# Performance work log

Hardware: AMD Instinct MI355X
Metric: run time of the kernel (lower is better)

Reference implementation:

```python
import jax, jax.numpy as jnp
import numpy as np

B, S, H_SZ = 1, 2048, 2048
E, K, KVH, D = 8, 2, 16, 128      # experts, top_k, kv heads, head_dim
QH = K * KVH                       # 32 query heads
QSZ = KVH * D                      # 2048 per-expert q/o size


def setup_inputs() -> dict:
    key = jax.random.key(0)
    ks = jax.random.split(key, 6)
    hidden_states = jax.random.normal(ks[0], (B, S, H_SZ), jnp.float32)
    causal = jnp.tril(jnp.ones((S, S), dtype=bool))
    attention_bias = jnp.where(causal, 0.0, -1e9).astype(jnp.float32)[None, None]  # [1,1,S,S]
    inv_freq = 1.0 / (10000.0 ** (jnp.arange(0, D, 2, dtype=jnp.float32) / D))     # [D/2]
    ang = jnp.arange(S, dtype=jnp.float32)[:, None] * inv_freq[None, :]            # [S,D/2]
    cos, sin = jnp.cos(ang), jnp.sin(ang)
    router_w = jax.random.normal(ks[1], (E, H_SZ), jnp.float32) * 0.02
    q_w = jax.random.normal(ks[2], (E, QSZ, H_SZ), jnp.float32) * 0.02
    o_w = jax.random.normal(ks[3], (E, H_SZ, QSZ), jnp.float32) * 0.02
    kv_w = jax.random.normal(ks[4], (2 * QSZ, H_SZ), jnp.float32) * 0.02
    bias = jax.random.normal(ks[5], (H_SZ,), jnp.float32) * 0.02
    return {"hidden_states": hidden_states, "attention_bias": attention_bias,
            "cos": cos, "sin": sin, "router_w": router_w, "q_w": q_w,
            "o_w": o_w, "kv_w": kv_w, "bias": bias}


def _rope(x, cos, sin):
    # x: [b,s,h,d]; half-rotation rotary, cos/sin: [s,d/2]
    d2 = x.shape[-1] // 2
    x1, x2 = x[..., :d2], x[..., d2:]
    c = cos[None, :, None, :]
    s = sin[None, :, None, :]
    return jnp.concatenate([x1 * c - x2 * s, x1 * s + x2 * c], axis=-1)


def reference(hidden_states, attention_bias, cos, sin, router_w, q_w, o_w, kv_w, bias):
    # ---- router: top-k + softmax over top-k logits ----
    logits = jnp.einsum('bsh,eh->bse', hidden_states, router_w)         # [b,s,E]
    top_vals, sel = jax.lax.top_k(logits, K)                            # [b,s,K]
    gates = jax.nn.softmax(top_vals, axis=-1)                           # [b,s,K]
    # ---- per-expert Q projections (dense, as in original), gather selected ----
    q_all = jnp.einsum('bsh,eqh->bseq', hidden_states, q_w)             # [b,s,E,QSZ]
    q_sel = jnp.take_along_axis(q_all, sel[..., None], axis=2)          # [b,s,K,QSZ]
    # slots -> kv-major head layout: [b,s,K,KVH,D] -> [b,s,KVH,K,D] -> [b,s,QH,D]
    q = q_sel.reshape(B, S, K, KVH, D).transpose(0, 1, 3, 2, 4).reshape(B, S, QH, D)
    # ---- shared K/V ----
    kv = jnp.einsum('bsh,oh->bso', hidden_states, kv_w)                 # [b,s,2*QSZ]
    k_st, v_st = jnp.split(kv, 2, axis=-1)
    k_st = k_st.reshape(B, S, KVH, D)
    v_st = v_st.reshape(B, S, KVH, D)
    # ---- rotary ----
    q = _rope(q, cos, sin)
    k_st = _rope(k_st, cos, sin)
    # ---- GQA attention (group size K; kv-major query layout matches repeat) ----
    k_rep = jnp.repeat(k_st, K, axis=2)                                 # [b,s,QH,D]
    v_rep = jnp.repeat(v_st, K, axis=2)
    scale = D ** -0.5
    scores = jnp.einsum('bqhd,bkhd->bhqk', q, k_rep) * scale + attention_bias
    probs = jax.nn.softmax(scores, axis=-1)
    attn = jnp.einsum('bhqk,bkhd->bqhd', probs, v_rep)                  # [b,s,QH,D]
    # back to slot-major: [b,s,KVH,K,D] -> [b,s,K,KVH,D] -> [b,s,K,QSZ]
    attn4 = attn.reshape(B, S, KVH, K, D).transpose(0, 1, 3, 2, 4).reshape(B, S, K, QSZ)
    # ---- per-expert O projections, masked + gated sum (as in original) ----
    out = jnp.zeros((B, S, H_SZ), hidden_states.dtype)
    for e in range(E):
        o_e = jnp.einsum('bskq,hq->bskh', attn4, o_w[e])                # [b,s,K,H]
        m = (sel == e).astype(hidden_states.dtype) * gates              # [b,s,K]
        out = out + jnp.einsum('bsk,bskh->bsh', m, o_e)
    return out + bias
```

## Files before the change

### kernel.cpp

```cpp
#include <hip/hip_runtime.h>
#include <hip/hip_bf16.h>
#include <stdint.h>

#define S_LEN 2048
#define HSZ 2048
#define NE 8
#define TOPK 2
#define NKVH 16
#define HD 128
#define NQH 32
#define QSZ 2048

typedef __attribute__((ext_vector_type(8))) __bf16 bf16x8;
typedef __attribute__((ext_vector_type(4))) float f32x4;

#define BM 128
#define BN 128
#define BK 64

__device__ __forceinline__ void gload_lds16(const void* g, void* l) {
  __builtin_amdgcn_global_load_lds((__attribute__((address_space(1))) void*)g,
                                   (__attribute__((address_space(3))) void*)l, 16, 0, 0);
}

__device__ __forceinline__ bf16x8 pack8(float4 a, float4 b) {
  bf16x8 r;
  r[0] = (__bf16)a.x; r[1] = (__bf16)a.y; r[2] = (__bf16)a.z; r[3] = (__bf16)a.w;
  r[4] = (__bf16)b.x; r[5] = (__bf16)b.y; r[6] = (__bf16)b.z; r[7] = (__bf16)b.w;
  return r;
}

__global__ __launch_bounds__(256) void cast_kernel(const float* __restrict__ src,
                                                   __bf16* __restrict__ dst, long n) {
  long i0 = ((long)blockIdx.x * 256 + threadIdx.x) * 4;
  long stride = (long)gridDim.x * 256 * 4;
  for (long i = i0; i < n; i += stride) {
    float4 v = *(const float4*)(src + i);
    unsigned short a = __builtin_bit_cast(unsigned short, (__bf16)v.x);
    unsigned short b = __builtin_bit_cast(unsigned short, (__bf16)v.y);
    unsigned short c = __builtin_bit_cast(unsigned short, (__bf16)v.z);
    unsigned short d = __builtin_bit_cast(unsigned short, (__bf16)v.w);
    uint2 o;
    o.x = (unsigned)a | ((unsigned)b << 16);
    o.y = (unsigned)c | ((unsigned)d << 16);
    *(uint2*)(dst + i) = o;
  }
}

__global__ __launch_bounds__(256) void router_kernel(const float* __restrict__ hs,
                                                     const float* __restrict__ rw,
                                                     int* __restrict__ sel,
                                                     float* __restrict__ gates) {
  const int s = blockIdx.x * 4 + (threadIdx.x >> 6);
  const int lane = threadIdx.x & 63;
  const float* row = hs + (size_t)s * HSZ;
  float acc[NE];
#pragma unroll
  for (int e = 0; e < NE; ++e) acc[e] = 0.f;
  for (int j = lane; j < HSZ; j += 64) {
    float x = row[j];
#pragma unroll
    for (int e = 0; e < NE; ++e) acc[e] += x * rw[e * HSZ + j];
  }
#pragma unroll
  for (int e = 0; e < NE; ++e) {
#pragma unroll
    for (int off = 32; off > 0; off >>= 1) acc[e] += __shfl_xor(acc[e], off);
  }
  if (lane == 0) {
    int i0 = 0; float v0 = acc[0];
#pragma unroll
    for (int e = 1; e < NE; ++e) if (acc[e] > v0) { v0 = acc[e]; i0 = e; }
    int i1 = -1; float v1 = -1e30f;
#pragma unroll
    for (int e = 0; e < NE; ++e) if (e != i0 && acc[e] > v1) { v1 = acc[e]; i1 = e; }
    float ge = __expf(v1 - v0);
    float den = 1.f + ge;
    sel[s * 2] = i0; sel[s * 2 + 1] = i1;
    gates[s * 2] = 1.f / den; gates[s * 2 + 1] = ge / den;
  }
}

__global__ void bucket_kernel(const int* __restrict__ sel, int* __restrict__ pair_list,
                              int* __restrict__ expert_off) {
  __shared__ int cnt[NE], base[NE];
  const int t = threadIdx.x;
  if (t < NE) cnt[t] = 0;
  __syncthreads();
  for (int p2 = t; p2 < S_LEN * TOPK; p2 += 256) atomicAdd(&cnt[sel[p2]], 1);
  __syncthreads();
  if (t == 0) {
    int run = 0;
#pragma unroll
    for (int e = 0; e < NE; ++e) { base[e] = run; expert_off[e] = run; run += cnt[e]; }
    expert_off[NE] = run;
  }
  __syncthreads();
  for (int p2 = t; p2 < S_LEN * TOPK; p2 += 256) {
    int pos = atomicAdd(&base[sel[p2]], 1);
    pair_list[pos] = p2;
  }
}

template <int MODE>
__global__ __launch_bounds__(256, 2) void gemm_kernel(const __bf16* __restrict__ A_src,
                                                      const float* __restrict__ B_src,
                                                      const int* __restrict__ pair_list,
                                                      const int* __restrict__ expert_off,
                                                      const float* __restrict__ gates,
                                                      __bf16* __restrict__ out_bf,
                                                      __bf16* __restrict__ out_vT,
                                                      float* __restrict__ out_f32) {
  constexpr int KD = 2048;
  constexpr int NT = KD / BK;
  const int n0 = blockIdx.x * BN;
  const int m0 = blockIdx.y * BM;
  const int e = blockIdx.z;
  int start = 0, cntv = S_LEN;
  if constexpr (MODE != 0) {
    start = expert_off[e];
    cntv = expert_off[e + 1] - start;
    if (m0 >= cntv) return;
  }
  const float* Bb = B_src + (size_t)e * QSZ * HSZ;
  __shared__ __attribute__((aligned(16))) __bf16 As[2][BM * BK];
  __shared__ __attribute__((aligned(16))) __bf16 Bs[2][BN * BK];
  __shared__ const __bf16* a_rows[BM];
  __shared__ int row_pair[BM];
  const int t = threadIdx.x;
  if (t < BM) {
    if constexpr (MODE == 0) {
      a_rows[t] = A_src + (size_t)(m0 + t) * KD;
      row_pair[t] = 0;
    } else {
      int idx = m0 + t;
      bool valid = idx < cntv;
      int pp = pair_list[start + (valid ? idx : 0)];
      row_pair[t] = valid ? pp : -1;
      size_t arow = (MODE == 1) ? (size_t)(pp >> 1) : (size_t)pp;
      a_rows[t] = A_src + arow * (size_t)KD;
    }
  }
  __syncthreads();

  const int lane = t & 63, w = t >> 6;
  const int wr = (w >> 1) * 64, wc = (w & 1) * 64;
  const int lr = lane & 15, g = lane >> 4;
  const int xa = lr & 7;

  const __bf16* a_srow[4];
  int a_soff[4];
#pragma unroll
  for (int i = 0; i < 4; ++i) {
    const int c = t + i * 256;
    const int row = c >> 3, win = c & 7;
    a_srow[i] = a_rows[row];
    a_soff[i] = (win ^ (row & 7)) * 8;
  }

  const int brow = t >> 2;
  const int bq = t & 3;
  const float* bp0 = Bb + (size_t)(n0 + brow) * KD + bq * 16;
  const float* bp1 = bp0 + (size_t)64 * KD;
  const int c0 = (2 * bq) ^ (brow & 7);
  const int c1 = (2 * bq + 1) ^ (brow & 7);
  const int bo00 = brow * BK + c0 * 8, bo01 = brow * BK + c1 * 8;
  const int bo10 = (brow + 64) * BK + c0 * 8, bo11 = (brow + 64) * BK + c1 * 8;

  f32x4 acc[4][4];
#pragma unroll
  for (int m = 0; m < 4; ++m)
#pragma unroll
    for (int n = 0; n < 4; ++n) acc[m][n] = (f32x4)0.f;

  float4 cA0 = *(const float4*)(bp0), cA1 = *(const float4*)(bp0 + 4);
  float4 cA2 = *(const float4*)(bp0 + 8), cA3 = *(const float4*)(bp0 + 12);
  float4 cB0 = *(const float4*)(bp1), cB1 = *(const float4*)(bp1 + 4);
  float4 cB2 = *(const float4*)(bp1 + 8), cB3 = *(const float4*)(bp1 + 12);
  __builtin_amdgcn_sched_barrier(0);
#pragma unroll
  for (int i = 0; i < 4; ++i)
    gload_lds16(a_srow[i] + a_soff[i], (char*)As[0] + (t + i * 256) * 16);
  __builtin_amdgcn_sched_barrier(0);

#pragma unroll 2
  for (int ti = 0; ti < NT; ++ti) {
    const int cur = ti & 1;
    *(bf16x8*)(&Bs[cur][bo00]) = pack8(cA0, cA1);
    *(bf16x8*)(&Bs[cur][bo01]) = pack8(cA2, cA3);
    *(bf16x8*)(&Bs[cur][bo10]) = pack8(cB0, cB1);
    *(bf16x8*)(&Bs[cur][bo11]) = pack8(cB2, cB3);
    asm volatile("s_waitcnt lgkmcnt(0)" ::: "memory");
    __builtin_amdgcn_s_barrier();

    if (ti + 1 < NT) {
      const int k1 = (ti + 1) * BK;
      cA0 = *(const float4*)(bp0 + k1); cA1 = *(const float4*)(bp0 + k1 + 4);
      cA2 = *(const float4*)(bp0 + k1 + 8); cA3 = *(const float4*)(bp0 + k1 + 12);
      cB0 = *(const float4*)(bp1 + k1); cB1 = *(const float4*)(bp1 + k1 + 4);
      cB2 = *(const float4*)(bp1 + k1 + 8); cB3 = *(const float4*)(bp1 + k1 + 12);
      __builtin_amdgcn_sched_barrier(0);
#pragma unroll
      for (int i = 0; i < 4; ++i)
        gload_lds16(a_srow[i] + k1 + a_soff[i], (char*)As[cur ^ 1] + (t + i * 256) * 16);
      asm volatile("s_waitcnt vmcnt(12)" ::: "memory");
    } else {
      asm volatile("s_waitcnt vmcnt(0)" ::: "memory");
    }
    __builtin_amdgcn_sched_barrier(0);

#pragma unroll
    for (int kk = 0; kk < BK; kk += 32) {
      bf16x8 af[4], bfv[4];
#pragma unroll
      for (int m = 0; m < 4; ++m)
        af[m] = *(const bf16x8*)(&As[cur][(wr + m * 16 + lr) * BK + (((kk >> 3) + g) ^ xa) * 8]);
#pragma unroll
      for (int n = 0; n < 4; ++n)
        bfv[n] = *(const bf16x8*)(&Bs[cur][(wc + n * 16 + lr) * BK + (((kk >> 3) + g) ^ xa) * 8]);
#pragma unroll
      for (int m = 0; m < 4; ++m)
#pragma unroll
        for (int n = 0; n < 4; ++n)
          acc[m][n] = __builtin_amdgcn_mfma_f32_16x16x32_bf16(af[m], bfv[n], acc[m][n], 0, 0, 0);
    }
    __builtin_amdgcn_sched_barrier(0);
  }

  const int lg = lane >> 4;
  if constexpr (MODE == 0) {
    if (n0 < 2048) {
#pragma unroll
      for (int m = 0; m < 4; ++m)
#pragma unroll
        for (int r = 0; r < 4; ++r) {
          const int row = wr + m * 16 + lg * 4 + r;
#pragma unroll
          for (int n = 0; n < 4; ++n) {
            const int col = n0 + wc + n * 16 + lr;
            out_bf[(size_t)(m0 + row) * 2048 + col] = (__bf16)acc[m][n][r];
          }
        }
    } else {
#pragma unroll
      for (int m = 0; m < 4; ++m) {
        const int sb = m0 + wr + m * 16 + lg * 4;
#pragma unroll
        for (int n = 0; n < 4; ++n) {
          const int cv = n0 + wc + n * 16 + lr - 2048;
          uint2 pk;
          unsigned short h0 = __builtin_bit_cast(unsigned short, (__bf16)acc[m][n][0]);
          unsigned short h1 = __builtin_bit_cast(unsigned short, (__bf16)acc[m][n][1]);
          unsigned short h2 = __builtin_bit_cast(unsigned short, (__bf16)acc[m][n][2]);
          unsigned short h3 = __builtin_bit_cast(unsigned short, (__bf16)acc[m][n][3]);
          pk.x = (unsigned)h0 | ((unsigned)h1 << 16);
          pk.y = (unsigned)h2 | ((unsigned)h3 << 16);
          *(uint2*)(out_vT + (size_t)cv * S_LEN + sb) = pk;
        }
      }
    }
  } else {
#pragma unroll
    for (int m = 0; m < 4; ++m) {
#pragma unroll
      for (int r = 0; r < 4; ++r) {
        const int row = wr + m * 16 + lg * 4 + r;
        const int pp = row_pair[row];
        if (pp < 0) continue;
        if constexpr (MODE == 1) {
#pragma unroll
          for (int n = 0; n < 4; ++n) {
            const int col = n0 + wc + n * 16 + lr;
            out_bf[(size_t)pp * QSZ + col] = (__bf16)acc[m][n][r];
          }
        } else {
          const float gt = gates[pp];
#pragma unroll
          for (int n = 0; n < 4; ++n) {
            const int col = n0 + wc + n * 16 + lr;
            out_f32[(size_t)pp * HSZ + col] = acc[m][n][r] * gt;
          }
        }
      }
    }
  }
}

__global__ __launch_bounds__(256) void rope_q_kernel(const __bf16* __restrict__ q_lin,
                                                     const float* __restrict__ cosb,
                                                     const float* __restrict__ sinb,
                                                     __bf16* __restrict__ q_attn) {
  const int idx = blockIdx.x * 4 + (threadIdx.x >> 6);
  const int lane = threadIdx.x & 63;
  const int s = idx >> 5;
  const int h = idx & 31;
  const int kvh = h >> 1, k = h & 1;
  const __bf16* src = q_lin + ((size_t)s * 2 + k) * QSZ + kvh * HD;
  float x1 = (float)src[lane];
  float x2 = (float)src[lane + 64];
  float c = cosb[s * 64 + lane], sn = sinb[s * 64 + lane];
  __bf16* dst = q_attn + ((size_t)h * S_LEN + s) * HD;
  dst[lane] = (__bf16)(x1 * c - x2 * sn);
  dst[lane + 64] = (__bf16)(x1 * sn + x2 * c);
}

__global__ __launch_bounds__(256) void rope_k_kernel(const __bf16* __restrict__ kv_lin,
                                                     const float* __restrict__ cosb,
                                                     const float* __restrict__ sinb,
                                                     __bf16* __restrict__ k_attn) {
  const int idx = blockIdx.x * 4 + (threadIdx.x >> 6);
  const int lane = threadIdx.x & 63;
  const int s = idx >> 4;
  const int gq = idx & 15;
  const __bf16* ksrc = kv_lin + (size_t)s * 2048 + gq * HD;
  float x1 = (float)ksrc[lane], x2 = (float)ksrc[lane + 64];
  float c = cosb[s * 64 + lane], sn = sinb[s * 64 + lane];
  __bf16* kd = k_attn + ((size_t)gq * S_LEN + s) * HD;
  kd[lane] = (__bf16)(x1 * c - x2 * sn);
  kd[lane + 64] = (__bf16)(x1 * sn + x2 * c);
}

__global__ __launch_bounds__(256, 2) void attn_kernel(const __bf16* __restrict__ q_attn,
                                                      const __bf16* __restrict__ k_attn,
                                                      const __bf16* __restrict__ vT,
                                                      __bf16* __restrict__ attn4) {
  __shared__ __attribute__((aligned(16))) __bf16 Ks[2][64 * 128];
  __shared__ __attribute__((aligned(16))) __bf16 Vs[2][128 * 64];
  const int h = blockIdx.x;
  const int by = (blockIdx.y < 8) ? blockIdx.y : 23 - blockIdx.y;
  const int s0 = by * 128;
  const int t = threadIdx.x;
  const int lane = t & 63;
  const int w = t >> 6;
  const int g = lane >> 4;
  const int lr = lane & 15;
  const int kvh = h >> 1;

  int koff[4], voff[4];
#pragma unroll
  for (int i = 0; i < 4; ++i) {
    const int c = t + i * 256;
    const int kvL = c >> 4, w16 = c & 15;
    koff[i] = kvL * HD + ((w16 ^ (kvL & 7)) * 8);
    const int d = c >> 3, w8 = c & 7;
    voff[i] = d * S_LEN + ((w8 ^ (d & 7)) * 8);
  }
  const __bf16* Kb = k_attn + (size_t)kvh * S_LEN * HD;
  const __bf16* Vb = vT + (size_t)kvh * HD * S_LEN;

  auto stage = [&](int buf, int kv0) {
#pragma unroll
    for (int i = 0; i < 4; ++i) {
      const int c = t + i * 256;
      gload_lds16(Kb + (size_t)kv0 * HD + koff[i], (char*)Ks[buf] + c * 16);
      gload_lds16(Vb + (size_t)kv0 + voff[i], (char*)Vs[buf] + c * 16);
    }
  };

  bf16x8 qf[2][4];
#pragma unroll
  for (int m = 0; m < 2; ++m) {
    const __bf16* qbase = q_attn + ((size_t)h * S_LEN + s0 + w * 32 + m * 16 + lr) * HD;
#pragma unroll
    for (int ds = 0; ds < 4; ++ds) qf[m][ds] = *(const bf16x8*)(qbase + ds * 32 + g * 8);
  }

  float m_run[2] = {-1e30f, -1e30f}, l_run[2] = {0.f, 0.f};
  f32x4 acc[2][8];
#pragma unroll
  for (int m = 0; m < 2; ++m)
#pragma unroll
    for (int dt = 0; dt < 8; ++dt) acc[m][dt] = (f32x4)0.f;

  const int xr = (lr & 7) << 4;
  const int nt = 2 * by + 2;
  stage(0, 0);
  for (int ti = 0; ti < nt; ++ti) {
    const int cur = ti & 1;
    const int kv0 = ti * 64;
    __syncthreads();
    if (ti + 1 < nt) stage(cur ^ 1, kv0 + 64);

    f32x4 sc[2][4];
#pragma unroll
    for (int m = 0; m < 2; ++m)
#pragma unroll
      for (int b = 0; b < 4; ++b) sc[m][b] = (f32x4)0.f;
#pragma unroll
    for (int b = 0; b < 4; ++b) {
#pragma unroll
      for (int ds = 0; ds < 4; ++ds) {
        const bf16x8 kf = *(const bf16x8*)((const char*)Ks[cur] +
            (b * 16 + lr) * 256 + ((ds * 64 + g * 16) ^ xr));
        sc[0][b] = __builtin_amdgcn_mfma_f32_16x16x32_bf16(kf, qf[0][ds], sc[0][b], 0, 0, 0);
        sc[1][b] = __builtin_amdgcn_mfma_f32_16x16x32_bf16(kf, qf[1][ds], sc[1][b], 0, 0, 0);
      }
    }

    bf16x8 paf[2][2];
#pragma unroll
    for (int m = 0; m < 2; ++m) {
      const int qrow = s0 + w * 32 + m * 16 + lr;
      float p[4][4];
      float tmax = -1e30f;
#pragma unroll
      for (int b = 0; b < 4; ++b)
#pragma unroll
        for (int r = 0; r < 4; ++r) {
          const int kv = kv0 + b * 16 + g * 4 + r;
          float v = sc[m][b][r] * 0.08838834764831845f;
          if (kv > qrow) v = -1e30f;
          p[b][r] = v;
          tmax = fmaxf(tmax, v);
        }
      tmax = fmaxf(tmax, __shfl_xor(tmax, 16));
      tmax = fmaxf(tmax, __shfl_xor(tmax, 32));
      const float m_new = fmaxf(m_run[m], tmax);
      const float alpha = __expf(m_run[m] - m_new);
      float lsum = 0.f;
#pragma unroll
      for (int b = 0; b < 4; ++b)
#pragma unroll
        for (int r = 0; r < 4; ++r) {
          p[b][r] = __expf(p[b][r] - m_new);
          lsum += p[b][r];
        }
      lsum += __shfl_xor(lsum, 16);
      lsum += __shfl_xor(lsum, 32);
      l_run[m] = l_run[m] * alpha + lsum;
      m_run[m] = m_new;

      float ar[4];
#pragma unroll
      for (int r = 0; r < 4; ++r) ar[r] = __shfl(alpha, g * 4 + r);
#pragma unroll
      for (int dt = 0; dt < 8; ++dt)
#pragma unroll
        for (int r = 0; r < 4; ++r) acc[m][dt][r] *= ar[r];

#pragma unroll
      for (int half = 0; half < 2; ++half) {
        bf16x8 af;
#pragma unroll
        for (int j = 0; j < 8; ++j) {
          const int srcl = lr + 16 * ((g & 1) * 2 + (j >> 2));
          const float va = __shfl(p[half * 2][j & 3], srcl);
          const float vb = __shfl(p[half * 2 + 1][j & 3], srcl);
          af[j] = (__bf16)((g >> 1) ? vb : va);
        }
        paf[m][half] = af;
      }
    }

#pragma unroll
    for (int dt = 0; dt < 8; ++dt) {
      const char* vrow = (const char*)Vs[cur] + (dt * 16 + lr) * 128;
      const bf16x8 v0 = *(const bf16x8*)(vrow + ((g * 16) ^ xr));
      const bf16x8 v1 = *(const bf16x8*)(vrow + ((64 + g * 16) ^ xr));
      acc[0][dt] = __builtin_amdgcn_mfma_f32_16x16x32_bf16(paf[0][0], v0, acc[0][dt], 0, 0, 0);
      acc[0][dt] = __builtin_amdgcn_mfma_f32_16x16x32_bf16(paf[0][1], v1, acc[0][dt], 0, 0, 0);
      acc[1][dt] = __builtin_amdgcn_mfma_f32_16x16x32_bf16(paf[1][0], v0, acc[1][dt], 0, 0, 0);
      acc[1][dt] = __builtin_amdgcn_mfma_f32_16x16x32_bf16(paf[1][1], v1, acc[1][dt], 0, 0, 0);
    }
  }

#pragma unroll
  for (int m = 0; m < 2; ++m) {
    const float li = 1.f / l_run[m];
    float linv[4];
#pragma unroll
    for (int r = 0; r < 4; ++r) linv[r] = __shfl(li, g * 4 + r);
#pragma unroll
    for (int dt = 0; dt < 8; ++dt)
#pragma unroll
      for (int r = 0; r < 4; ++r) {
        const int qg = s0 + w * 32 + m * 16 + g * 4 + r;
        attn4[((size_t)qg * 2 + (h & 1)) * QSZ + kvh * HD + dt * 16 + lr] =
            (__bf16)(acc[m][dt][r] * linv[r]);
      }
  }
}

__global__ __launch_bounds__(256) void final_kernel(const float* __restrict__ o_tmp,
                                                    const float* __restrict__ bias,
                                                    float* __restrict__ out) {
  const size_t i = ((size_t)blockIdx.x * 256 + threadIdx.x) * 4;
  const int s = (int)(i >> 11);
  const int hcol = (int)(i & 2047);
  float4 a = *(const float4*)(o_tmp + ((size_t)s * 2) * HSZ + hcol);
  float4 b = *(const float4*)(o_tmp + ((size_t)s * 2 + 1) * HSZ + hcol);
  float4 bb = *(const float4*)(bias + hcol);
  float4 o;
  o.x = a.x + b.x + bb.x; o.y = a.y + b.y + bb.y;
  o.z = a.z + b.z + bb.z; o.w = a.w + b.w + bb.w;
  *(float4*)(out + i) = o;
}

extern "C" void kernel_launch(void* const* d_in, const int* in_sizes, int n_in,
                              void* d_out, int out_size, void* d_ws, size_t ws_size,
                              hipStream_t stream) {
  (void)in_sizes; (void)n_in; (void)out_size; (void)ws_size;
  const float* hs = (const float*)d_in[0];
  const float* cosb = (const float*)d_in[2];
  const float* sinb = (const float*)d_in[3];
  const float* rw = (const float*)d_in[4];
  const float* qw = (const float*)d_in[5];
  const float* ow = (const float*)d_in[6];
  const float* kvw = (const float*)d_in[7];
  const float* bias = (const float*)d_in[8];
  float* outp = (float*)d_out;

  char* base = (char*)d_ws;
  size_t off = 0;
  auto take = [&](size_t bytes) {
    char* r = base + off;
    off += (bytes + 255) & ~(size_t)255;
    return r;
  };
  __bf16* hid_bf  = (__bf16*)take((size_t)S_LEN * HSZ * 2);
  __bf16* k_attn  = (__bf16*)take((size_t)NKVH * S_LEN * HD * 2);
  __bf16* v_attnT = (__bf16*)take((size_t)NKVH * HD * S_LEN * 2);
  char* bufA = take((size_t)S_LEN * 4096 * 2);
  char* bufBC = take((size_t)S_LEN * TOPK * HSZ * 4);
  int* sel = (int*)take((size_t)S_LEN * TOPK * 4);
  float* gates = (float*)take((size_t)S_LEN * TOPK * 4);
  int* pair_list = (int*)take((size_t)S_LEN * TOPK * 4);
  int* expert_off = (int*)take((size_t)(NE + 1) * 4);

  __bf16* kv_lin = (__bf16*)bufA;
  __bf16* attn4 = (__bf16*)bufA;
  __bf16* q_lin = (__bf16*)bufBC;
  __bf16* q_attn = (__bf16*)(bufBC + (size_t)16 * 1024 * 1024);
  float* o_tmp = (float*)bufBC;

  cast_kernel<<<1024, 256, 0, stream>>>(hs, hid_bf, (long)S_LEN * HSZ);
  router_kernel<<<S_LEN / 4, 256, 0, stream>>>(hs, rw, sel, gates);
  bucket_kernel<<<1, 256, 0, stream>>>(sel, pair_list, expert_off);
  gemm_kernel<0><<<dim3(4096 / BN, S_LEN / BM, 1), 256, 0, stream>>>(
      hid_bf, kvw, nullptr, nullptr, nullptr, kv_lin, v_attnT, nullptr);
  rope_k_kernel<<<S_LEN * NKVH / 4, 256, 0, stream>>>(kv_lin, cosb, sinb, k_attn);
  gemm_kernel<1><<<dim3(QSZ / BN, 32, NE), 256, 0, stream>>>(
      hid_bf, qw, pair_list, expert_off, nullptr, q_lin, nullptr, nullptr);
  rope_q_kernel<<<S_LEN * NQH / 4, 256, 0, stream>>>(q_lin, cosb, sinb, q_attn);
  attn_kernel<<<dim3(NQH, 16), 256, 0, stream>>>(q_attn, k_attn, v_attnT, attn4);
  gemm_kernel<2><<<dim3(HSZ / BN, 32, NE), 256, 0, stream>>>(
      attn4, ow, pair_list, expert_off, gates, nullptr, nullptr, o_tmp);
  final_kernel<<<(S_LEN * HSZ / 4) / 256, 256, 0, stream>>>(o_tmp, bias, outp);
}
```

Measured before the change: 423.5 us.

## Split-K expert GEMMs, fuse Q rotary into attention, emit bf16 partials

The two expert GEMMs now split the K dimension in two across blockIdx.z and write bf16 partial results. The Q partials are summed and rotated inside the attention kernel, which removes the separate rope_q pass. The O partials are summed in the final kernel, so the fp32 o_tmp buffer is no longer needed. The GEMM tile depth drops from 64 to 32 and launch bounds ask for 4 blocks per SM to raise occupancy, at the cost of dropping the LDS XOR swizzle and the explicit vmcnt waits. The bf16 partial sums lose some precision, and the unswizzled layout may cause LDS bank conflicts.

```diff
diff --git a/kernel.cpp b/kernel.cpp
--- a/kernel.cpp
+++ b/kernel.cpp
@@ -16,7 +16,7 @@
 
 #define BM 128
 #define BN 128
-#define BK 64
+#define BK 32
 
 __device__ __forceinline__ void gload_lds16(const void* g, void* l) {
   __builtin_amdgcn_global_load_lds((__attribute__((address_space(1))) void*)g,
@@ -103,26 +103,26 @@
 }
 
 template <int MODE>
-__global__ __launch_bounds__(256, 2) void gemm_kernel(const __bf16* __restrict__ A_src,
-                                                      const float* __restrict__ B_src,
-                                                      const int* __restrict__ pair_list,
-                                                      const int* __restrict__ expert_off,
-                                                      const float* __restrict__ gates,
-                                                      __bf16* __restrict__ out_bf,
-                                                      __bf16* __restrict__ out_vT,
-                                                      float* __restrict__ out_f32) {
+__global__ __launch_bounds__(256, 4) void gemm_kernel(
+    const __bf16* __restrict__ A_src, const float* __restrict__ B_src,
+    const int* __restrict__ pair_list, const int* __restrict__ expert_off,
+    const float* __restrict__ gates, __bf16* __restrict__ out0,
+    __bf16* __restrict__ out_vT) {
   constexpr int KD = 2048;
-  constexpr int NT = KD / BK;
+  constexpr int NT = (MODE == 0) ? 64 : 32;
   const int n0 = blockIdx.x * BN;
   const int m0 = blockIdx.y * BM;
-  const int e = blockIdx.z;
-  int start = 0, cntv = S_LEN;
+  int kbase = 0, kz = 0, start = 0, cntv = S_LEN;
+  const float* Bb = B_src;
   if constexpr (MODE != 0) {
+    const int e = blockIdx.z >> 1;
+    kz = blockIdx.z & 1;
+    kbase = kz * 1024;
     start = expert_off[e];
     cntv = expert_off[e + 1] - start;
     if (m0 >= cntv) return;
-  }
-  const float* Bb = B_src + (size_t)e * QSZ * HSZ;
+    Bb = B_src + (size_t)e * QSZ * HSZ;
+  }
   __shared__ __attribute__((aligned(16))) __bf16 As[2][BM * BK];
   __shared__ __attribute__((aligned(16))) __bf16 Bs[2][BN * BK];
   __shared__ const __bf16* a_rows[BM];
@@ -138,7 +138,7 @@
       int pp = pair_list[start + (valid ? idx : 0)];
       row_pair[t] = valid ? pp : -1;
       size_t arow = (MODE == 1) ? (size_t)(pp >> 1) : (size_t)pp;
-      a_rows[t] = A_src + arow * (size_t)KD;
+      a_rows[t] = A_src + arow * (size_t)KD + kbase;
     }
   }
   __syncthreads();
@@ -146,26 +146,18 @@
   const int lane = t & 63, w = t >> 6;
   const int wr = (w >> 1) * 64, wc = (w & 1) * 64;
   const int lr = lane & 15, g = lane >> 4;
-  const int xa = lr & 7;
-
-  const __bf16* a_srow[4];
-  int a_soff[4];
-#pragma unroll
-  for (int i = 0; i < 4; ++i) {
+
+  const __bf16* a_srow[2];
+  int a_scol[2];
+#pragma unroll
+  for (int i = 0; i < 2; ++i) {
     const int c = t + i * 256;
-    const int row = c >> 3, win = c & 7;
-    a_srow[i] = a_rows[row];
-    a_soff[i] = (win ^ (row & 7)) * 8;
-  }
-
-  const int brow = t >> 2;
-  const int bq = t & 3;
-  const float* bp0 = Bb + (size_t)(n0 + brow) * KD + bq * 16;
-  const float* bp1 = bp0 + (size_t)64 * KD;
-  const int c0 = (2 * bq) ^ (brow & 7);
-  const int c1 = (2 * bq + 1) ^ (brow & 7);
-  const int bo00 = brow * BK + c0 * 8, bo01 = brow * BK + c1 * 8;
-  const int bo10 = (brow + 64) * BK + c0 * 8, bo11 = (brow + 64) * BK + c1 * 8;
+    a_srow[i] = a_rows[c >> 2];
+    a_scol[i] = (c & 3) * 8;
+  }
+
+  const float* bp = Bb + (size_t)(n0 + (t >> 1)) * KD + kbase + (t & 1) * 16;
+  const int bwo = (t >> 1) * BK + (t & 1) * 16;
 
   f32x4 acc[4][4];
 #pragma unroll
@@ -173,51 +165,42 @@
 #pragma unroll
     for (int n = 0; n < 4; ++n) acc[m][n] = (f32x4)0.f;
 
-  float4 cA0 = *(const float4*)(bp0), cA1 = *(const float4*)(bp0 + 4);
-  float4 cA2 = *(const float4*)(bp0 + 8), cA3 = *(const float4*)(bp0 + 12);
-  float4 cB0 = *(const float4*)(bp1), cB1 = *(const float4*)(bp1 + 4);
-  float4 cB2 = *(const float4*)(bp1 + 8), cB3 = *(const float4*)(bp1 + 12);
-  __builtin_amdgcn_sched_barrier(0);
-#pragma unroll
-  for (int i = 0; i < 4; ++i)
-    gload_lds16(a_srow[i] + a_soff[i], (char*)As[0] + (t + i * 256) * 16);
+  auto stageA = [&](int buf, int k0) {
+#pragma unroll
+    for (int i = 0; i < 2; ++i)
+      gload_lds16(a_srow[i] + k0 + a_scol[i], (char*)As[buf] + (t + i * 256) * 16);
+  };
+
+  float4 c0, c1, c2, c3;
+#define B_LOAD(KB)                                                           \
+  c0 = *(const float4*)(bp + (KB));     c1 = *(const float4*)(bp + (KB) + 4); \
+  c2 = *(const float4*)(bp + (KB) + 8); c3 = *(const float4*)(bp + (KB) + 12);
+
+  stageA(0, 0);
+  B_LOAD(0)
   __builtin_amdgcn_sched_barrier(0);
 
 #pragma unroll 2
   for (int ti = 0; ti < NT; ++ti) {
     const int cur = ti & 1;
-    *(bf16x8*)(&Bs[cur][bo00]) = pack8(cA0, cA1);
-    *(bf16x8*)(&Bs[cur][bo01]) = pack8(cA2, cA3);
-    *(bf16x8*)(&Bs[cur][bo10]) = pack8(cB0, cB1);
-    *(bf16x8*)(&Bs[cur][bo11]) = pack8(cB2, cB3);
+    *(bf16x8*)(&Bs[cur][bwo]) = pack8(c0, c1);
+    *(bf16x8*)(&Bs[cur][bwo + 8]) = pack8(c2, c3);
     asm volatile("s_waitcnt lgkmcnt(0)" ::: "memory");
     __builtin_amdgcn_s_barrier();
-
+    __builtin_amdgcn_sched_barrier(0);
     if (ti + 1 < NT) {
-      const int k1 = (ti + 1) * BK;
-      cA0 = *(const float4*)(bp0 + k1); cA1 = *(const float4*)(bp0 + k1 + 4);
-      cA2 = *(const float4*)(bp0 + k1 + 8); cA3 = *(const float4*)(bp0 + k1 + 12);
-      cB0 = *(const float4*)(bp1 + k1); cB1 = *(const float4*)(bp1 + k1 + 4);
-      cB2 = *(const float4*)(bp1 + k1 + 8); cB3 = *(const float4*)(bp1 + k1 + 12);
-      __builtin_amdgcn_sched_barrier(0);
-#pragma unroll
-      for (int i = 0; i < 4; ++i)
-        gload_lds16(a_srow[i] + k1 + a_soff[i], (char*)As[cur ^ 1] + (t + i * 256) * 16);
-      asm volatile("s_waitcnt vmcnt(12)" ::: "memory");
-    } else {
-      asm volatile("s_waitcnt vmcnt(0)" ::: "memory");
+      stageA(cur ^ 1, (ti + 1) * BK);
+      B_LOAD((ti + 1) * BK)
     }
     __builtin_amdgcn_sched_barrier(0);
-
-#pragma unroll
-    for (int kk = 0; kk < BK; kk += 32) {
+    {
       bf16x8 af[4], bfv[4];
 #pragma unroll
       for (int m = 0; m < 4; ++m)
-        af[m] = *(const bf16x8*)(&As[cur][(wr + m * 16 + lr) * BK + (((kk >> 3) + g) ^ xa) * 8]);
+        af[m] = *(const bf16x8*)(&As[cur][(wr + m * 16 + lr) * BK + g * 8]);
 #pragma unroll
       for (int n = 0; n < 4; ++n)
-        bfv[n] = *(const bf16x8*)(&Bs[cur][(wc + n * 16 + lr) * BK + (((kk >> 3) + g) ^ xa) * 8]);
+        bfv[n] = *(const bf16x8*)(&Bs[cur][(wc + n * 16 + lr) * BK + g * 8]);
 #pragma unroll
       for (int m = 0; m < 4; ++m)
 #pragma unroll
@@ -226,6 +209,7 @@
     }
     __builtin_amdgcn_sched_barrier(0);
   }
+#undef B_LOAD
 
   const int lg = lane >> 4;
   if constexpr (MODE == 0) {
@@ -238,7 +222,7 @@
 #pragma unroll
           for (int n = 0; n < 4; ++n) {
             const int col = n0 + wc + n * 16 + lr;
-            out_bf[(size_t)(m0 + row) * 2048 + col] = (__bf16)acc[m][n][r];
+            out0[(size_t)(m0 + row) * 2048 + col] = (__bf16)acc[m][n][r];
           }
         }
     } else {
@@ -260,6 +244,7 @@
       }
     }
   } else {
+    __bf16* outp = out0 + (size_t)kz * 4096 * 2048;
 #pragma unroll
     for (int m = 0; m < 4; ++m) {
 #pragma unroll
@@ -267,41 +252,16 @@
         const int row = wr + m * 16 + lg * 4 + r;
         const int pp = row_pair[row];
         if (pp < 0) continue;
-        if constexpr (MODE == 1) {
-#pragma unroll
-          for (int n = 0; n < 4; ++n) {
-            const int col = n0 + wc + n * 16 + lr;
-            out_bf[(size_t)pp * QSZ + col] = (__bf16)acc[m][n][r];
-          }
-        } else {
-          const float gt = gates[pp];
-#pragma unroll
-          for (int n = 0; n < 4; ++n) {
-            const int col = n0 + wc + n * 16 + lr;
-            out_f32[(size_t)pp * HSZ + col] = acc[m][n][r] * gt;
-          }
+        float gt = 1.f;
+        if constexpr (MODE == 2) gt = gates[pp];
+#pragma unroll
+        for (int n = 0; n < 4; ++n) {
+          const int col = n0 + wc + n * 16 + lr;
+          outp[(size_t)pp * 2048 + col] = (__bf16)(acc[m][n][r] * gt);
         }
       }
     }
   }
-}
-
-__global__ __launch_bounds__(256) void rope_q_kernel(const __bf16* __restrict__ q_lin,
-                                                     const float* __restrict__ cosb,
-                                                     const float* __restrict__ sinb,
-                                                     __bf16* __restrict__ q_attn) {
-  const int idx = blockIdx.x * 4 + (threadIdx.x >> 6);
-  const int lane = threadIdx.x & 63;
-  const int s = idx >> 5;
-  const int h = idx & 31;
-  const int kvh = h >> 1, k = h & 1;
-  const __bf16* src = q_lin + ((size_t)s * 2 + k) * QSZ + kvh * HD;
-  float x1 = (float)src[lane];
-  float x2 = (float)src[lane + 64];
-  float c = cosb[s * 64 + lane], sn = sinb[s * 64 + lane];
-  __bf16* dst = q_attn + ((size_t)h * S_LEN + s) * HD;
-  dst[lane] = (__bf16)(x1 * c - x2 * sn);
-  dst[lane + 64] = (__bf16)(x1 * sn + x2 * c);
 }
 
 __global__ __launch_bounds__(256) void rope_k_kernel(const __bf16* __restrict__ kv_lin,
@@ -320,9 +280,11 @@
   kd[lane + 64] = (__bf16)(x1 * sn + x2 * c);
 }
 
-__global__ __launch_bounds__(256, 2) void attn_kernel(const __bf16* __restrict__ q_attn,
+__global__ __launch_bounds__(256, 2) void attn_kernel(const __bf16* __restrict__ q_part,
                                                       const __bf16* __restrict__ k_attn,
                                                       const __bf16* __restrict__ vT,
+                                                      const float* __restrict__ cosb,
+                                                      const float* __restrict__ sinb,
                                                       __bf16* __restrict__ attn4) {
   __shared__ __attribute__((aligned(16))) __bf16 Ks[2][64 * 128];
   __shared__ __attribute__((aligned(16))) __bf16 Vs[2][128 * 64];
@@ -360,9 +322,29 @@
   bf16x8 qf[2][4];
 #pragma unroll
   for (int m = 0; m < 2; ++m) {
-    const __bf16* qbase = q_attn + ((size_t)h * S_LEN + s0 + w * 32 + m * 16 + lr) * HD;
-#pragma unroll
-    for (int ds = 0; ds < 4; ++ds) qf[m][ds] = *(const bf16x8*)(qbase + ds * 32 + g * 8);
+    const int qrow = s0 + w * 32 + m * 16 + lr;
+    const __bf16* p0 = q_part + (size_t)(qrow * 2 + (h & 1)) * QSZ + kvh * HD;
+    const __bf16* p1 = p0 + (size_t)4096 * 2048;
+    const float* cp = cosb + qrow * 64;
+    const float* sp = sinb + qrow * 64;
+#pragma unroll
+    for (int ds = 0; ds < 4; ++ds) {
+      const int d0 = ds * 32 + g * 8;
+      const int dl = d0 & 63;
+      const bf16x8 xa = *(const bf16x8*)(p0 + d0);
+      const bf16x8 xb = *(const bf16x8*)(p1 + d0);
+      const bf16x8 ya = *(const bf16x8*)(p0 + (d0 ^ 64));
+      const bf16x8 yb = *(const bf16x8*)(p1 + (d0 ^ 64));
+      bf16x8 o;
+#pragma unroll
+      for (int j = 0; j < 8; ++j) {
+        const float x = (float)xa[j] + (float)xb[j];
+        const float y = (float)ya[j] + (float)yb[j];
+        const float c = cp[dl + j], sn = sp[dl + j];
+        o[j] = (__bf16)((ds < 2) ? (x * c - y * sn) : (y * sn + x * c));
+      }
+      qf[m][ds] = o;
+    }
   }
 
   float m_run[2] = {-1e30f, -1e30f}, l_run[2] = {0.f, 0.f};
@@ -481,19 +463,23 @@
   }
 }
 
-__global__ __launch_bounds__(256) void final_kernel(const float* __restrict__ o_tmp,
+__global__ __launch_bounds__(256) void final_kernel(const __bf16* __restrict__ o_part,
                                                     const float* __restrict__ bias,
                                                     float* __restrict__ out) {
   const size_t i = ((size_t)blockIdx.x * 256 + threadIdx.x) * 4;
   const int s = (int)(i >> 11);
   const int hcol = (int)(i & 2047);
-  float4 a = *(const float4*)(o_tmp + ((size_t)s * 2) * HSZ + hcol);
-  float4 b = *(const float4*)(o_tmp + ((size_t)s * 2 + 1) * HSZ + hcol);
-  float4 bb = *(const float4*)(bias + hcol);
-  float4 o;
-  o.x = a.x + b.x + bb.x; o.y = a.y + b.y + bb.y;
-  o.z = a.z + b.z + bb.z; o.w = a.w + b.w + bb.w;
-  *(float4*)(out + i) = o;
+  float4 r = *(const float4*)(bias + hcol);
+#pragma unroll
+  for (int idx = 0; idx < 4; ++idx) {
+    const size_t row = (size_t)(idx >> 1) * 4096 + 2 * s + (idx & 1);
+    const ushort4 u = *(const ushort4*)(o_part + row * HSZ + hcol);
+    r.x += (float)__builtin_bit_cast(__bf16, u.x);
+    r.y += (float)__builtin_bit_cast(__bf16, u.y);
+    r.z += (float)__builtin_bit_cast(__bf16, u.z);
+    r.w += (float)__builtin_bit_cast(__bf16, u.w);
+  }
+  *(float4*)(out + i) = r;
 }
 
 extern "C" void kernel_launch(void* const* d_in, const int* in_sizes, int n_in,
@@ -521,7 +507,7 @@
   __bf16* k_attn  = (__bf16*)take((size_t)NKVH * S_LEN * HD * 2);
   __bf16* v_attnT = (__bf16*)take((size_t)NKVH * HD * S_LEN * 2);
   char* bufA = take((size_t)S_LEN * 4096 * 2);
-  char* bufBC = take((size_t)S_LEN * TOPK * HSZ * 4);
+  char* bufBC = take((size_t)2 * 4096 * HSZ * 2);
   int* sel = (int*)take((size_t)S_LEN * TOPK * 4);
   float* gates = (float*)take((size_t)S_LEN * TOPK * 4);
   int* pair_list = (int*)take((size_t)S_LEN * TOPK * 4);
@@ -529,21 +515,19 @@
 
   __bf16* kv_lin = (__bf16*)bufA;
   __bf16* attn4 = (__bf16*)bufA;
-  __bf16* q_lin = (__bf16*)bufBC;
-  __bf16* q_attn = (__bf16*)(bufBC + (size_t)16 * 1024 * 1024);
-  float* o_tmp = (float*)bufBC;
+  __bf16* q_part = (__bf16*)bufBC;
+  __bf16* o_part = (__bf16*)bufBC;
 
   cast_kernel<<<1024, 256, 0, stream>>>(hs, hid_bf, (long)S_LEN * HSZ);
   router_kernel<<<S_LEN / 4, 256, 0, stream>>>(hs, rw, sel, gates);
   bucket_kernel<<<1, 256, 0, stream>>>(sel, pair_list, expert_off);
   gemm_kernel<0><<<dim3(4096 / BN, S_LEN / BM, 1), 256, 0, stream>>>(
-      hid_bf, kvw, nullptr, nullptr, nullptr, kv_lin, v_attnT, nullptr);
+      hid_bf, kvw, nullptr, nullptr, nullptr, kv_lin, v_attnT);
   rope_k_kernel<<<S_LEN * NKVH / 4, 256, 0, stream>>>(kv_lin, cosb, sinb, k_attn);
-  gemm_kernel<1><<<dim3(QSZ / BN, 32, NE), 256, 0, stream>>>(
-      hid_bf, qw, pair_list, expert_off, nullptr, q_lin, nullptr, nullptr);
-  rope_q_kernel<<<S_LEN * NQH / 4, 256, 0, stream>>>(q_lin, cosb, sinb, q_attn);
-  attn_kernel<<<dim3(NQH, 16), 256, 0, stream>>>(q_attn, k_attn, v_attnT, attn4);
-  gemm_kernel<2><<<dim3(HSZ / BN, 32, NE), 256, 0, stream>>>(
-      attn4, ow, pair_list, expert_off, gates, nullptr, nullptr, o_tmp);
-  final_kernel<<<(S_LEN * HSZ / 4) / 256, 256, 0, stream>>>(o_tmp, bias, outp);
-}
+  gemm_kernel<1><<<dim3(QSZ / BN, 16, NE * 2), 256, 0, stream>>>(
+      hid_bf, qw, pair_list, expert_off, nullptr, q_part, nullptr);
+  attn_kernel<<<dim3(NQH, 16), 256, 0, stream>>>(q_part, k_attn, v_attnT, cosb, sinb, attn4);
+  gemm_kernel<2><<<dim3(HSZ / BN, 16, NE * 2), 256, 0, stream>>>(
+      attn4, ow, pair_list, expert_off, gates, o_part, nullptr);
+  final_kernel<<<(S_LEN * HSZ / 4) / 256, 256, 0, stream>>>(o_part, bias, outp);
+}
```

New measurement: 431.7 us. Within noise of the previous version (+1.9%).
